# Optimization experiments

Measured on AMD Instinct MI355X. Metric: run time of the kernel, lower is better.

Reference implementation:

```python
import jax, jax.numpy as jnp
import numpy as np

N = 2060          # drug-graph nodes (m_drug_d_num)
F_OUT = 901       # out_feats, forced by Linear(901*2, ...)
M = 901 + (N - 1183)  # 1778 fused node rows
E = N * 64
N_TRAIN, N_TEST = 100000, 30000
EPS = 1e-5


def setup_inputs() -> dict:
    key = jax.random.key(0)
    ks = jax.random.split(key, 30)
    f32 = jnp.float32
    inp = {
        'x_feat': jax.random.normal(ks[0], (N, N), f32),
        'mirna_feat': jax.random.normal(ks[1], (M, F_OUT), f32),
        'Wg': jax.random.normal(ks[2], (N, F_OUT), f32) * 0.02,
        'att_src': jax.random.normal(ks[3], (F_OUT,), f32) * 0.05,
        'att_dst': jax.random.normal(ks[4], (F_OUT,), f32) * 0.05,
        'gat_b': jnp.zeros((F_OUT,), f32),
        'lw1': jax.random.normal(ks[5], (1, 2), f32) * 0.5,
        'lb1': jnp.zeros((1,), f32),
        'lw2': jax.random.normal(ks[6], (2, 1), f32) * 0.5,
        'lb2': jnp.zeros((2,), f32),
        'gw1': jax.random.normal(ks[7], (1, 2), f32) * 0.5,
        'gb1': jnp.zeros((1,), f32),
        'gw2': jax.random.normal(ks[8], (2, 1), f32) * 0.5,
        'gb2': jnp.zeros((2,), f32),
        'W1': jax.random.normal(ks[9], (2 * F_OUT, 1024), f32) * 0.02,
        'b1': jnp.zeros((1024,), f32),
        'W2': jax.random.normal(ks[10], (1024, 512), f32) * 0.03,
        'b2': jnp.zeros((512,), f32),
        'W3': jax.random.normal(ks[11], (512, 64), f32) * 0.04,
        'b3': jnp.zeros((64,), f32),
        'W4': jax.random.normal(ks[12], (64, 1), f32) * 0.1,
        'b4': jnp.zeros((1,), f32),
        'edge_index': jax.random.randint(ks[13], (2, E), 0, N, jnp.int32),
        'train_sample': jax.random.randint(ks[14], (N_TRAIN, 2), 0, M, jnp.int32),
        'test_sample': jax.random.randint(ks[15], (N_TEST, 2), 0, M, jnp.int32),
    }
    return inp


def _bn(x, axes):
    # BatchNorm in train mode (fresh module: gamma=1, beta=0, biased batch var)
    mu = x.mean(axes, keepdims=True)
    var = x.var(axes, keepdims=True)
    return (x - mu) * jax.lax.rsqrt(var + EPS)


def _gat(x, Wg, att_src, att_dst, gat_b, edge_index):
    # single-head PyG-style GATConv with self loops, negative_slope=0.2
    h = x @ Wg                                         # [N, F]
    loop = jnp.arange(N, dtype=edge_index.dtype)
    src = jnp.concatenate([edge_index[0], loop])
    dst = jnp.concatenate([edge_index[1], loop])
    a_s = h @ att_src                                  # [N]
    a_d = h @ att_dst
    e = jax.nn.leaky_relu(a_s[src] + a_d[dst], 0.2)    # per-edge logits
    emax = jax.ops.segment_max(e, dst, num_segments=N)
    ex = jnp.exp(e - emax[dst])
    denom = jax.ops.segment_sum(ex, dst, num_segments=N)
    alpha = ex / denom[dst]
    out = jax.ops.segment_sum(alpha[:, None] * h[src], dst, num_segments=N) + gat_b
    return jax.nn.relu(out)                            # F.relu in MGL (MGC relu is idempotent)


def _forward(x_feat, mirna_feat, Wg, att_src, att_dst, gat_b,
             lw1, lb1, lw2, lb2, gw1, gb1, gw2, gb2,
             W1, b1, W2, b2, W3, b3, W4, b4,
             edge_index, train_sample, test_sample):
    g = _gat(x_feat, Wg, att_src, att_dst, gat_b, edge_index)      # [N, 901]
    drug_view = jnp.concatenate([g[:901], g[1183:]], axis=0)       # [M, 901]
    x = jnp.stack([drug_view, mirna_feat], axis=1)                 # [M, 2, 901]  (B=M, C=2, H=1 dropped, W=901)

    # MS_CAM (channels=2, r=2), BN in train mode
    xl = jnp.einsum('mcw,oc->mow', x, lw1) + lb1[None, :, None]    # [M, 1, 901]
    xl = jax.nn.relu(_bn(xl, (0, 2)))
    xl = jnp.einsum('mcw,oc->mow', xl, lw2) + lb2[None, :, None]   # [M, 2, 901]
    xl = _bn(xl, (0, 2))

    gp = x.mean(axis=2)                                            # [M, 2] global avg pool
    xg = gp @ gw1.T + gb1                                          # [M, 1]
    xg = jax.nn.relu(_bn(xg, (0,)))
    xg = xg @ gw2.T + gb2                                          # [M, 2]
    xg = _bn(xg, (0,))

    wei = jax.nn.sigmoid(xl + xg[:, :, None])
    x = x * wei                                                    # [M, 2, 901]
    fused = (x[:, 0, :] + x[:, 1, :]) * 0.5                        # [M, 901]

    def score(pairs):
        emb = jnp.concatenate([fused[pairs[:, 0]], fused[pairs[:, 1]]], axis=1)  # [B, 1802]
        h = emb @ W1 + b1
        h = h @ W2 + b2
        h = h @ W3 + b3
        return jax.nn.sigmoid(h @ W4 + b4)

    return score(train_sample), score(test_sample)


def reference(x_feat, mirna_feat, Wg, att_src, att_dst, gat_b,
              lw1, lb1, lw2, lb2, gw1, gb1, gw2, gb2,
              W1, b1, W2, b2, W3, b3, W4, b4,
              edge_index, train_sample, test_sample):
    return _forward(x_feat, mirna_feat, Wg, att_src, att_dst, gat_b,
                    lw1, lb1, lw2, lb2, gw1, gb1, gw2, gb2,
                    W1, b1, W2, b2, W3, b3, W4, b4,
                    edge_index, train_sample, test_sample)
```

## Files before the change

kernel.cpp:

```cpp
#include <hip/hip_runtime.h>

typedef unsigned short u16;
typedef unsigned int   u32;

#define NN   2060
#define FF   901
#define HP   904
#define MM   1778
#define EE   131840
#define ETOT 133900
#define NTR  100000
#define NOUT 130000
#define MP   2112
#define KP   2080
#define NP   960
#define EPSV 1e-5f
#define NTOT 1601978.0

typedef __attribute__((ext_vector_type(4))) float f32x4;
typedef __attribute__((ext_vector_type(8))) short bf16x8;

#define GLL16(g,l) __builtin_amdgcn_global_load_lds( \
    (const __attribute__((address_space(1))) u32*)(g), \
    (__attribute__((address_space(3))) u32*)(l), 16, 0, 0)

__device__ __forceinline__ float bf2f(u16 u){ return __uint_as_float(((u32)u)<<16); }
__device__ __forceinline__ u16 f2bf(float f){
  u32 b = __float_as_uint(f);
  return (u16)((b + 0x7fffu + ((b>>16)&1u)) >> 16);
}
__device__ __forceinline__ float ldf(const void* p, size_t i, int bf){
  return bf ? bf2f(((const u16*)p)[i]) : ((const float*)p)[i];
}
__device__ __forceinline__ u16 ldb(const void* p, size_t i, int bf){
  return bf ? ((const u16*)p)[i] : f2bf(((const float*)p)[i]);
}
__device__ __forceinline__ float waveSum(float v){
  #pragma unroll
  for (int o = 32; o; o >>= 1) v += __shfl_down(v, o);
  return v;
}
__device__ __forceinline__ int waveSumI(int v){
  #pragma unroll
  for (int o = 32; o; o >>= 1) v += __shfl_down(v, o);
  return v;
}
__device__ __forceinline__ int flagWave(const u32* __restrict__ x){
  int l = threadIdx.x & 63;
  u32 w0 = x[l], w1 = x[l + 64];
  int big = (((w0 >> 7)  & 0xFFu) >= 0xC0u) + (((w0 >> 23) & 0xFFu) >= 0xC0u)
          + (((w1 >> 7)  & 0xFFu) >= 0xC0u) + (((w1 >> 23) & 0xFFu) >= 0xC0u);
  big = waveSumI(big);
  return (__shfl(big, 0) >= 8) ? 0 : 1;
}
__device__ __forceinline__ void edgeSD(const int* __restrict__ ei, int e, int& src, int& dst){
  if (e < EE){ src = ei[e]; dst = ei[EE + e]; } else { src = dst = e - EE; }
}

__global__ __launch_bounds__(256) void pad_k(const void* __restrict__ X, const void* __restrict__ Wg,
                                             const void* __restrict__ W3, const void* __restrict__ W4,
                                             const void* __restrict__ b3, const void* __restrict__ b4,
                                             const int* __restrict__ ei,
                                             u16* __restrict__ Ap, u16* __restrict__ BT,
                                             float* __restrict__ u3, float* __restrict__ cp,
                                             int* __restrict__ cnts, int* bfp){
  __shared__ u16 tt[32][33];
  int bf = flagWave((const u32*)X);
  int blk = blockIdx.x, tid = threadIdx.x;
  if (blk == 0 && tid == 0) *bfp = bf;
  if (blk < MP){
    int row = blk;
    for (int c0 = tid * 8; c0 < KP; c0 += 2048){
      u16 v[8] = {0,0,0,0,0,0,0,0};
      if (row < NN){
        if (c0 + 8 <= NN){
          if (bf){
            ushort4 t0 = *(const ushort4*)((const u16*)X + (size_t)row * NN + c0);
            ushort4 t1 = *(const ushort4*)((const u16*)X + (size_t)row * NN + c0 + 4);
            v[0]=t0.x; v[1]=t0.y; v[2]=t0.z; v[3]=t0.w;
            v[4]=t1.x; v[5]=t1.y; v[6]=t1.z; v[7]=t1.w;
          } else {
            float4 t0 = *(const float4*)((const float*)X + (size_t)row * NN + c0);
            float4 t1 = *(const float4*)((const float*)X + (size_t)row * NN + c0 + 4);
            v[0]=f2bf(t0.x); v[1]=f2bf(t0.y); v[2]=f2bf(t0.z); v[3]=f2bf(t0.w);
            v[4]=f2bf(t1.x); v[5]=f2bf(t1.y); v[6]=f2bf(t1.z); v[7]=f2bf(t1.w);
          }
        } else {
          #pragma unroll
          for (int i = 0; i < 8; ++i)
            if (c0 + i < NN) v[i] = ldb(X, (size_t)row * NN + c0 + i, bf);
        }
      }
      *(uint4*)(Ap + (size_t)row * KP + c0) = *(const uint4*)v;
    }
  } else if (blk < MP + 1950){
    int t = blk - MP;
    int kb = (t % 65) * 32, nb = (t / 65) * 32;
    int tx = tid & 31, ty = tid >> 5;
    #pragma unroll
    for (int i = 0; i < 4; ++i){
      int k = kb + ty + 8*i, n = nb + tx;
      u16 v = 0;
      if (k < NN && n < FF) v = ldb(Wg, (size_t)k * FF + n, bf);
      tt[ty + 8*i][tx] = v;
    }
    __syncthreads();
    #pragma unroll
    for (int i = 0; i < 4; ++i){
      int n = nb + ty + 8*i, k = kb + tx;
      if (n < NP && k < KP) BT[(size_t)n * KP + k] = tt[tx][ty + 8*i];
    }
  } else if (blk < MP + 1950 + 514){
    if (tid >= 64) return;
    int ob = blk - (MP + 1950);
    if (ob > 512) return;
    float s = (ob < 512) ? ldf(W3, (size_t)ob*64 + tid, bf) * ldf(W4, tid, bf)
                         : ldf(b3, tid, bf) * ldf(W4, tid, bf);
    s = waveSum(s);
    if (tid == 0){ if (ob < 512) u3[ob] = s; else cp[0] = s + ldf(b4, 0, bf); }
  } else {
    int e = (blk - (MP + 1950 + 514)) * 256 + tid;
    if (e >= ETOT) return;
    int src, dst; edgeSD(ei, e, src, dst);
    atomicAdd(&cnts[dst], 1);
  }
}

__global__ __launch_bounds__(256) void scan_k(const int* __restrict__ counts, int* __restrict__ offs,
                                              const void* __restrict__ W2, const void* __restrict__ b2,
                                              const float* __restrict__ u3, float* __restrict__ u2,
                                              float* __restrict__ cp, const int* bfp){
  int blk = blockIdx.x, tid = threadIdx.x;
  if (blk == 0){
    __shared__ int part[256];
    const int CH = (NN + 255) / 256;
    int base = tid * CH, s = 0;
    for (int i = 0; i < CH; ++i){ int idx = base + i; if (idx < NN) s += counts[idx]; }
    part[tid] = s;
    __syncthreads();
    if (tid == 0){ int run = 0; for (int i = 0; i < 256; ++i){ int v = part[i]; part[i] = run; run += v; } }
    __syncthreads();
    int run = part[tid];
    for (int i = 0; i < CH; ++i){ int idx = base + i; if (idx < NN){ offs[idx] = run; run += counts[idx]; } }
    if (tid == 255) offs[NN] = run;
  } else {
    int bf = *bfp;
    __shared__ float sh[4];
    #pragma unroll 1
    for (int r = 0; r < 2; ++r){
      int ob = (blk - 1) * 2 + r;
      if (ob <= 1024){
        float s = 0;
        if (ob < 1024){ for (int j = tid; j < 512; j += 256) s += ldf(W2, (size_t)ob*512 + j, bf) * u3[j]; }
        else          { for (int j = tid; j < 512; j += 256) s += ldf(b2, j, bf) * u3[j]; }
        s = waveSum(s);
        __syncthreads();
        if ((tid & 63) == 0) sh[tid >> 6] = s;
        __syncthreads();
        if (tid == 0){ float t = sh[0]+sh[1]+sh[2]+sh[3]; if (ob < 1024) u2[ob] = t; else cp[1] = t; }
      }
    }
  }
}

__global__ __launch_bounds__(256) void gemm_k(const u16* __restrict__ A, const u16* __restrict__ BT,
                                              u16* __restrict__ h,
                                              const void* __restrict__ W1, const void* __restrict__ b1,
                                              const float* __restrict__ u2, float* __restrict__ u1,
                                              float* __restrict__ cp, const int* bfp){
  __shared__ __align__(16) u16 sA[2][64*32];
  __shared__ __align__(16) u16 sB[2][64*32];
  __shared__ float shr[4];
  int blk = blockIdx.x, tid = threadIdx.x;
  if (blk >= 495){
    int bf = *bfp;
    #pragma unroll 1
    for (int r = 0; r < 4; ++r){
      int ob = (blk - 495) * 4 + r;
      if (ob <= 1802){
        float s = 0;
        if (ob < 1802){ for (int j = tid; j < 1024; j += 256) s += ldf(W1, (size_t)ob*1024 + j, bf) * u2[j]; }
        else          { for (int j = tid; j < 1024; j += 256) s += ldf(b1, j, bf) * u2[j]; }
        s = waveSum(s);
        __syncthreads();
        if ((tid & 63) == 0) shr[tid >> 6] = s;
        __syncthreads();
        if (tid == 0){ float t = shr[0]+shr[1]+shr[2]+shr[3]; if (ob < 1802) u1[ob] = t; else cp[2] = t; }
      }
    }
    return;
  }
  int bm = (blk % 33) * 64, bn = (blk / 33) * 64;
  int lane = tid & 63, wave = tid >> 6;
  int wm = (wave >> 1) * 32, wn = (wave & 1) * 32;
  f32x4 acc[2][2] = {};
  int srow = tid >> 2;
  int schunk = (tid & 3) ^ ((tid >> 3) & 3);
  const u16* gA = A  + (size_t)(bm + srow) * KP + schunk * 8;
  const u16* gB = BT + (size_t)(bn + srow) * KP + schunk * 8;
  int fr = lane & 15, quad = lane >> 4;
  int qs = quad ^ ((fr >> 1) & 3);
  const int KIT = KP / 32;
  GLL16(gA, &sA[0][wave * 512]);
  GLL16(gB, &sB[0][wave * 512]);
  for (int kt = 0; kt < KIT; ++kt){
    int cur = kt & 1;
    __syncthreads();
    if (kt + 1 < KIT){
      GLL16(gA + (kt + 1) * 32, &sA[cur ^ 1][wave * 512]);
      GLL16(gB + (kt + 1) * 32, &sB[cur ^ 1][wave * 512]);
    }
    bf16x8 a0 = *(const bf16x8*)&sA[cur][(wm      + fr) * 32 + qs * 8];
    bf16x8 a1 = *(const bf16x8*)&sA[cur][(wm + 16 + fr) * 32 + qs * 8];
    bf16x8 b0 = *(const bf16x8*)&sB[cur][(wn      + fr) * 32 + qs * 8];
    bf16x8 b1 = *(const bf16x8*)&sB[cur][(wn + 16 + fr) * 32 + qs * 8];
    acc[0][0] = __builtin_amdgcn_mfma_f32_16x16x32_bf16(a0, b0, acc[0][0], 0,0,0);
    acc[0][1] = __builtin_amdgcn_mfma_f32_16x16x32_bf16(a0, b1, acc[0][1], 0,0,0);
    acc[1][0] = __builtin_amdgcn_mfma_f32_16x16x32_bf16(a1, b0, acc[1][0], 0,0,0);
    acc[1][1] = __builtin_amdgcn_mfma_f32_16x16x32_bf16(a1, b1, acc[1][1], 0,0,0);
  }
  #pragma unroll
  for (int im = 0; im < 2; ++im)
    #pragma unroll
    for (int in = 0; in < 2; ++in)
      #pragma unroll
      for (int i = 0; i < 4; ++i){
        int row = bm + wm + im*16 + quad*4 + i;
        int col = bn + wn + in*16 + fr;
        if (row < NN && col < FF) h[(size_t)row * HP + col] = f2bf(acc[im][in][i]);
      }
}

__global__ __launch_bounds__(256) void asd_k(const u16* __restrict__ h, const void* att_s, const void* att_d,
                                             float* a_s, float* a_d, const int* bfp){
  int bf = *bfp;
  int wv = threadIdx.x >> 6, lane = threadIdx.x & 63;
  int n = blockIdx.x * 4 + wv;
  if (n >= NN) return;
  float ss = 0, sd = 0;
  for (int f = lane; f < FF; f += 64){
    float hv = bf2f(h[(size_t)n * HP + f]);
    ss += hv * ldf(att_s, f, bf);
    sd += hv * ldf(att_d, f, bf);
  }
  ss = waveSum(ss); sd = waveSum(sd);
  if (lane == 0){ a_s[n] = ss; a_d[n] = sd; }
}

__global__ __launch_bounds__(256) void edge2_k(const int* __restrict__ ei, const float* __restrict__ a_s,
                                               const float* __restrict__ a_d, float* __restrict__ denom,
                                               const int* __restrict__ offs, int* __restrict__ fill,
                                               int* __restrict__ csr_src, float* __restrict__ csr_w){
  int e = blockIdx.x * 256 + threadIdx.x;
  if (e >= ETOT) return;
  int src, dst; edgeSD(ei, e, src, dst);
  float x = a_s[src] + a_d[dst];
  float ev = x > 0.f ? x : 0.2f * x;
  float ex = expf(ev);
  atomicAdd(&denom[dst], ex);
  int pos = offs[dst] + atomicAdd(&fill[dst], 1);
  csr_src[pos] = src; csr_w[pos] = ex;
}

__device__ __forceinline__ void acc8(float* a, uint4 v, float w){
  u32 arr[4] = {v.x, v.y, v.z, v.w};
  #pragma unroll
  for (int i = 0; i < 4; ++i){
    a[2*i]   += w * __uint_as_float((arr[i] & 0xFFFFu) << 16);
    a[2*i+1] += w * __uint_as_float(arr[i] & 0xFFFF0000u);
  }
}
__global__ __launch_bounds__(128) void aggr_k(const u16* __restrict__ h, const int* __restrict__ offs,
                                              const int* __restrict__ csr_src, const float* __restrict__ csr_w,
                                              const float* __restrict__ denom, const void* gat_b,
                                              const void* __restrict__ mirna,
                                              const void* lw1, const void* lb1,
                                              float* __restrict__ g, float* __restrict__ gp,
                                              float2* __restrict__ pA, const int* bfp){
  int bf = *bfp;
  int m = blockIdx.x, tid = threadIdx.x;
  int dst = m < 901 ? m : m + 282;
  int o0 = offs[dst], o1 = offs[dst + 1];
  float inv = 1.0f / denom[dst];
  __shared__ int   sS[128];
  __shared__ float sW[128];
  __shared__ float red[4][2];
  const int c = tid;
  float a[8] = {0,0,0,0,0,0,0,0};
  for (int base = o0; base < o1; base += 128){
    int nb = min(128, o1 - base);
    __syncthreads();
    if (tid < nb){ sS[tid] = csr_src[base + tid]; sW[tid] = csr_w[base + tid] * inv; }
    __syncthreads();
    if (c < 113){
      int k = 0;
      for (; k + 4 <= nb; k += 4){
        int   i0 = sS[k], i1 = sS[k+1], i2 = sS[k+2], i3 = sS[k+3];
        float w0 = sW[k], w1 = sW[k+1], w2 = sW[k+2], w3 = sW[k+3];
        uint4 v0 = ((const uint4*)(h + (size_t)i0 * HP))[c];
        uint4 v1 = ((const uint4*)(h + (size_t)i1 * HP))[c];
        uint4 v2 = ((const uint4*)(h + (size_t)i2 * HP))[c];
        uint4 v3 = ((const uint4*)(h + (size_t)i3 * HP))[c];
        acc8(a, v0, w0); acc8(a, v1, w1); acc8(a, v2, w2); acc8(a, v3, w3);
      }
      for (; k < nb; ++k){
        uint4 v0 = ((const uint4*)(h + (size_t)sS[k] * HP))[c];
        acc8(a, v0, sW[k]);
      }
    }
  }
  float w00 = ldf(lw1,0,bf), w01 = ldf(lw1,1,bf), bb = ldf(lb1,0,bf);
  float sx0 = 0, sx1 = 0, sl = 0, sl2 = 0;
  if (c < 113){
    int f0 = 8 * c;
    float r[8];
    #pragma unroll
    for (int i = 0; i < 8; ++i){
      bool inb = (f0 + i) < FF;
      float v = a[i] + (inb ? ldf(gat_b, f0 + i, bf) : 0.f);
      v = v > 0.f ? v : 0.f;
      r[i] = inb ? v : 0.f;
      if (inb){
        float x1 = ldf(mirna, (size_t)m * FF + f0 + i, bf);
        float xl = w00*r[i] + w01*x1 + bb;
        sx0 += r[i]; sx1 += x1; sl += xl; sl2 += xl*xl;
      }
    }
    float4* go = (float4*)(g + (size_t)dst * HP);
    go[2*c]   = make_float4(r[0], r[1], r[2], r[3]);
    go[2*c+1] = make_float4(r[4], r[5], r[6], r[7]);
  }
  sx0 = waveSum(sx0); sx1 = waveSum(sx1); sl = waveSum(sl); sl2 = waveSum(sl2);
  int wv = tid >> 6;
  if ((tid & 63) == 0){ red[0][wv]=sx0; red[1][wv]=sx1; red[2][wv]=sl; red[3][wv]=sl2; }
  __syncthreads();
  if (tid == 0){
    gp[2*m]   = (red[0][0]+red[0][1]) / (float)FF;
    gp[2*m+1] = (red[1][0]+red[1][1]) / (float)FF;
    pA[m] = make_float2(red[2][0]+red[2][1], red[3][0]+red[3][1]);
  }
}

__global__ __launch_bounds__(256) void xg_k(const float* __restrict__ gp, const void* gw1, const void* gb1,
                                            const void* gw2, float* __restrict__ xg2b,
                                            const float2* __restrict__ pA, double* __restrict__ Sd,
                                            const int* bfp){
  int bf = *bfp;
  __shared__ float xs[MM];
  __shared__ float red[2][4];
  __shared__ float bc[3];
  int tid = threadIdx.x;
  float s = 0, s2 = 0;
  for (int m = tid; m < MM; m += 256){ float2 p = pA[m]; s += p.x; s2 += p.y; }
  s = waveSum(s); s2 = waveSum(s2);
  if ((tid & 63) == 0){ red[0][tid>>6] = s; red[1][tid>>6] = s2; }
  __syncthreads();
  if (tid == 0){
    Sd[0] = (double)(red[0][0]+red[0][1]+red[0][2]+red[0][3]);
    Sd[1] = (double)(red[1][0]+red[1][1]+red[1][2]+red[1][3]);
  }
  __syncthreads();
  float g10 = ldf(gw1,0,bf), g11 = ldf(gw1,1,bf), b1v = ldf(gb1,0,bf);
  s = 0; s2 = 0;
  for (int m = tid; m < MM; m += 256){
    float v = g10*gp[2*m] + g11*gp[2*m+1] + b1v;
    xs[m] = v; s += v; s2 += v*v;
  }
  s = waveSum(s); s2 = waveSum(s2);
  __syncthreads();
  if ((tid & 63) == 0){ red[0][tid>>6] = s; red[1][tid>>6] = s2; }
  __syncthreads();
  if (tid == 0){
    float t  = red[0][0]+red[0][1]+red[0][2]+red[0][3];
    float t2 = red[1][0]+red[1][1]+red[1][2]+red[1][3];
    float mean = t / (float)MM, var = t2 / (float)MM - mean*mean;
    bc[0] = mean; bc[1] = rsqrtf(var + EPSV);
  }
  __syncthreads();
  float mean = bc[0], rs = bc[1];
  s = 0; s2 = 0;
  for (int m = tid; m < MM; m += 256){
    float r = (xs[m] - mean) * rs; r = r > 0.f ? r : 0.f;
    xs[m] = r; s += r; s2 += r*r;
  }
  s = waveSum(s); s2 = waveSum(s2);
  __syncthreads();
  if ((tid & 63) == 0){ red[0][tid>>6] = s; red[1][tid>>6] = s2; }
  __syncthreads();
  if (tid == 0){
    float t  = red[0][0]+red[0][1]+red[0][2]+red[0][3];
    float t2 = red[1][0]+red[1][1]+red[1][2]+red[1][3];
    float mrg = t / (float)MM, vrg = t2 / (float)MM - mrg*mrg;
    float g20 = ldf(gw2,0,bf), g21 = ldf(gw2,1,bf);
    bc[0] = mrg;
    bc[1] = g20 * rsqrtf(g20*g20*vrg + EPSV);
    bc[2] = g21 * rsqrtf(g21*g21*vrg + EPSV);
  }
  __syncthreads();
  float mrg = bc[0], c0 = bc[1], c1 = bc[2];
  for (int m = tid; m < MM; m += 256){
    float d = xs[m] - mrg;
    xg2b[2*m] = c0 * d; xg2b[2*m+1] = c1 * d;
  }
}

__global__ __launch_bounds__(256) void statsB_k(const float* __restrict__ g, const void* __restrict__ mirna,
                                                const void* lw1, const void* lb1,
                                                const double* __restrict__ S, float2* __restrict__ pB,
                                                const int* bfp){
  int bf = *bfp;
  int m = blockIdx.x, tid = threadIdx.x;
  int gr = m < 901 ? m : m + 282;
  float w00 = ldf(lw1,0,bf), w01 = ldf(lw1,1,bf), bb = ldf(lb1,0,bf);
  float mu1 = (float)(S[0] / NTOT);
  float rs1 = rsqrtf((float)(S[1] / NTOT) - mu1*mu1 + EPSV);
  float sr = 0, sr2 = 0;
  for (int w = tid; w < FF; w += 256){
    float x0 = g[(size_t)gr * HP + w];
    float x1 = ldf(mirna, (size_t)m * FF + w, bf);
    float xl = w00*x0 + w01*x1 + bb;
    float r = (xl - mu1) * rs1; r = r > 0.f ? r : 0.f;
    sr += r; sr2 += r*r;
  }
  sr = waveSum(sr); sr2 = waveSum(sr2);
  __shared__ float sh[2][4];
  if ((tid & 63) == 0){ sh[0][tid>>6] = sr; sh[1][tid>>6] = sr2; }
  __syncthreads();
  if (tid == 0) pB[m] = make_float2(sh[0][0]+sh[0][1]+sh[0][2]+sh[0][3],
                                    sh[1][0]+sh[1][1]+sh[1][2]+sh[1][3]);
}

__global__ __launch_bounds__(256) void redB_k(const float2* __restrict__ pB, double* __restrict__ Sd){
  int tid = threadIdx.x;
  float s = 0, s2 = 0;
  for (int m = tid; m < MM; m += 256){ float2 p = pB[m]; s += p.x; s2 += p.y; }
  s = waveSum(s); s2 = waveSum(s2);
  __shared__ float sh[2][4];
  if ((tid & 63) == 0){ sh[0][tid>>6] = s; sh[1][tid>>6] = s2; }
  __syncthreads();
  if (tid == 0){
    Sd[2] = (double)(sh[0][0]+sh[0][1]+sh[0][2]+sh[0][3]);
    Sd[3] = (double)(sh[1][0]+sh[1][1]+sh[1][2]+sh[1][3]);
  }
}

__global__ __launch_bounds__(256) void fs_k(const float* __restrict__ g, const void* __restrict__ mirna,
                                            const void* lw1, const void* lb1, const void* lw2,
                                            const double* __restrict__ S, const float* __restrict__ xg2b,
                                            const float* __restrict__ u1,
                                            float* __restrict__ s0, float* __restrict__ s1, const int* bfp){
  int bf = *bfp;
  int m = blockIdx.x, tid = threadIdx.x;
  int gr = m < 901 ? m : m + 282;
  float w00 = ldf(lw1,0,bf), w01 = ldf(lw1,1,bf), bb = ldf(lb1,0,bf);
  float mu1 = (float)(S[0] / NTOT);
  float rs1 = rsqrtf((float)(S[1] / NTOT) - mu1*mu1 + EPSV);
  float mr  = (float)(S[2] / NTOT);
  float vr  = (float)(S[3] / NTOT) - mr*mr;
  float l20 = ldf(lw2,0,bf), l21 = ldf(lw2,1,bf);
  float A0 = l20 * rsqrtf(l20*l20*vr + EPSV);
  float A1 = l21 * rsqrtf(l21*l21*vr + EPSV);
  float xa = xg2b[2*m], xb = xg2b[2*m+1];
  float p0 = 0, p1 = 0;
  for (int w = tid; w < FF; w += 256){
    float x0 = g[(size_t)gr * HP + w];
    float x1 = ldf(mirna, (size_t)m * FF + w, bf);
    float xl = w00*x0 + w01*x1 + bb;
    float r = (xl - mu1) * rs1; r = r > 0.f ? r : 0.f;
    float rc = r - mr;
    float z0 = A0*rc + xa, z1 = A1*rc + xb;
    float sg0 = 1.f / (1.f + expf(-z0));
    float sg1 = 1.f / (1.f + expf(-z1));
    float f = 0.5f * (x0*sg0 + x1*sg1);
    p0 += f * u1[w]; p1 += f * u1[901 + w];
  }
  p0 = waveSum(p0); p1 = waveSum(p1);
  __shared__ float sh[2][4];
  if ((tid & 63) == 0){ sh[0][tid>>6] = p0; sh[1][tid>>6] = p1; }
  __syncthreads();
  if (tid == 0){
    s0[m] = sh[0][0]+sh[0][1]+sh[0][2]+sh[0][3];
    s1[m] = sh[1][0]+sh[1][1]+sh[1][2]+sh[1][3];
  }
}

__global__ __launch_bounds__(256) void out_k(const int* __restrict__ tr, const int* __restrict__ te,
                                             const float* __restrict__ s0, const float* __restrict__ s1,
                                             const float* __restrict__ cp, void* __restrict__ out,
                                             const int* bfp){
  int bf = *bfp;
  int b = blockIdx.x * 256 + threadIdx.x;
  if (b >= NOUT) return;
  int i, j;
  if (b < NTR){ i = tr[2*b]; j = tr[2*b + 1]; }
  else { int t = b - NTR; i = te[2*t]; j = te[2*t + 1]; }
  float z = s0[i] + s1[j] + cp[0] + cp[1] + cp[2];
  float v = 1.f / (1.f + expf(-z));
  if (bf) ((u16*)out)[b] = f2bf(v);
  else    ((float*)out)[b] = v;
}

extern "C" void kernel_launch(void* const* d_in, const int* in_sizes, int n_in,
                              void* d_out, int out_size, void* d_ws, size_t ws_size,
                              hipStream_t stream){
  const void* x_feat = d_in[0];
  const void* mirna  = d_in[1];
  const void* Wg     = d_in[2];
  const void* att_s  = d_in[3];
  const void* att_d  = d_in[4];
  const void* gat_b  = d_in[5];
  const void* lw1    = d_in[6];
  const void* lb1    = d_in[7];
  const void* lw2    = d_in[8];
  const void* gw1    = d_in[10];
  const void* gb1    = d_in[11];
  const void* gw2    = d_in[12];
  const void* W1     = d_in[14];
  const void* b1     = d_in[15];
  const void* W2     = d_in[16];
  const void* b2     = d_in[17];
  const void* W3     = d_in[18];
  const void* b3     = d_in[19];
  const void* W4     = d_in[20];
  const void* b4     = d_in[21];
  const int* ei      = (const int*)d_in[22];
  const int* tr      = (const int*)d_in[23];
  const int* te      = (const int*)d_in[24];

  char* ws = (char*)d_ws;
  size_t off = 0;
  auto alloc = [&](size_t bytes)->size_t{ size_t o = off; off += (bytes + 255) & ~(size_t)255; return o; };
  size_t oA  = alloc((size_t)MP*KP*2);
  size_t oBT = alloc((size_t)NP*KP*2);
  size_t oH  = alloc((size_t)NN*HP*2);
  size_t oCS = alloc((size_t)ETOT*4);
  size_t oCW = alloc((size_t)ETOT*4);
  size_t oAS = alloc(NN*4);
  size_t oAD = alloc(NN*4);
  size_t oOF = alloc((NN+1)*4);
  size_t oGP = alloc(MM*2*4);
  size_t oXG = alloc(MM*2*4);
  size_t oS0 = alloc(MM*4);
  size_t oS1 = alloc(MM*4);
  size_t oU3 = alloc(512*4);
  size_t oU2 = alloc(1024*4);
  size_t oU1 = alloc(1802*4);
  size_t oPA = alloc(MM*8);
  size_t oPB = alloc(MM*8);
  size_t oSS = alloc(4*8);
  size_t oCP = alloc(3*4);
  size_t oBF = alloc(4);
  size_t zstart = off;
  size_t oCT = alloc(NN*4);
  size_t oFL = alloc(NN*4);
  size_t oDN = alloc(NN*4);
  size_t zend = off;

  u16*   Ap   = (u16*)(ws+oA);
  u16*   BT   = (u16*)(ws+oBT);
  u16*   h    = (u16*)(ws+oH);
  float* gbuf = (float*)(ws+oA);
  int*   csrS = (int*)(ws+oCS);
  float* csrW = (float*)(ws+oCW);
  float* a_s  = (float*)(ws+oAS);
  float* a_d  = (float*)(ws+oAD);
  int*   offs = (int*)(ws+oOF);
  float* gp   = (float*)(ws+oGP);
  float* xg2b = (float*)(ws+oXG);
  float* s0   = (float*)(ws+oS0);
  float* s1   = (float*)(ws+oS1);
  float* u3   = (float*)(ws+oU3);
  float* u2   = (float*)(ws+oU2);
  float* u1   = (float*)(ws+oU1);
  float2* pA  = (float2*)(ws+oPA);
  float2* pB  = (float2*)(ws+oPB);
  double* Sd  = (double*)(ws+oSS);
  float* cp   = (float*)(ws+oCP);
  int*   bfp  = (int*)(ws+oBF);
  int*   cnts = (int*)(ws+oCT);
  int*   fill = (int*)(ws+oFL);
  float* denom= (float*)(ws+oDN);

  hipMemsetAsync(ws + zstart, 0, zend - zstart, stream);

  pad_k  <<<MP + 1950 + 514 + (ETOT+255)/256, 256, 0, stream>>>(
      x_feat, Wg, W3, W4, b3, b4, ei, Ap, BT, u3, cp, cnts, bfp);
  scan_k <<<514, 256, 0, stream>>>(cnts, offs, W2, b2, u3, u2, cp, bfp);
  gemm_k <<<495 + 451, 256, 0, stream>>>(Ap, BT, h, W1, b1, u2, u1, cp, bfp);
  asd_k  <<<(NN+3)/4, 256, 0, stream>>>(h, att_s, att_d, a_s, a_d, bfp);
  edge2_k<<<(ETOT+255)/256, 256, 0, stream>>>(ei, a_s, a_d, denom, offs, fill, csrS, csrW);
  aggr_k <<<MM, 128, 0, stream>>>(h, offs, csrS, csrW, denom, gat_b, mirna, lw1, lb1, gbuf, gp, pA, bfp);
  xg_k   <<<1, 256, 0, stream>>>(gp, gw1, gb1, gw2, xg2b, pA, Sd, bfp);
  statsB_k<<<MM, 256, 0, stream>>>(gbuf, mirna, lw1, lb1, Sd, pB, bfp);
  redB_k <<<1, 256, 0, stream>>>(pB, Sd);
  fs_k   <<<MM, 256, 0, stream>>>(gbuf, mirna, lw1, lb1, lw2, Sd, xg2b, u1, s0, s1, bfp);
  out_k  <<<(NOUT+255)/256, 256, 0, stream>>>(tr, te, s0, s1, cp, d_out, bfp);
}
```

Baseline: 259.4 us.

## Merge small tail and mid kernels into persistent kernels with grid barriers

Replaces the asd/edge kernels and the five tail kernels (xg, statsB, redB, fs, out) with two persistent 512-block kernels. They use a software grid barrier built on atomics. The tail kernel keeps each block's g and mirna rows in shared memory across phases, so they are not re-read from global memory. This removes several launch gaps and one global re-read. It risks deadlock if all 512 blocks are not co-resident, and the barrier spin adds latency.

```diff
diff --git a/kernel.cpp b/kernel.cpp
--- a/kernel.cpp
+++ b/kernel.cpp
@@ -16,6 +16,7 @@
 #define NP   960
 #define EPSV 1e-5f
 #define NTOT 1601978.0
+#define GRD  512
 
 typedef __attribute__((ext_vector_type(4))) float f32x4;
 typedef __attribute__((ext_vector_type(8))) short bf16x8;
@@ -55,6 +56,26 @@
 }
 __device__ __forceinline__ void edgeSD(const int* __restrict__ ei, int e, int& src, int& dst){
   if (e < EE){ src = ei[e]; dst = ei[EE + e]; } else { src = dst = e - EE; }
+}
+
+__device__ __forceinline__ void gbar(int* cnt, int* gen){
+  __syncthreads();
+  if (threadIdx.x == 0){
+    __threadfence();
+    int g = atomicAdd(gen, 0);
+    if (atomicAdd(cnt, 1) == GRD - 1){
+      atomicExch(cnt, 0);
+      __threadfence();
+      atomicAdd(gen, 1);
+    } else {
+      for (long it = 0; it < (1L << 22); ++it){
+        if (atomicAdd(gen, 0) != g) break;
+        __builtin_amdgcn_s_sleep(8);
+      }
+    }
+    __threadfence();
+  }
+  __syncthreads();
 }
 
 __global__ __launch_bounds__(256) void pad_k(const void* __restrict__ X, const void* __restrict__ Wg,
@@ -231,35 +252,36 @@
       }
 }
 
-__global__ __launch_bounds__(256) void asd_k(const u16* __restrict__ h, const void* att_s, const void* att_d,
-                                             float* a_s, float* a_d, const int* bfp){
-  int bf = *bfp;
-  int wv = threadIdx.x >> 6, lane = threadIdx.x & 63;
-  int n = blockIdx.x * 4 + wv;
-  if (n >= NN) return;
-  float ss = 0, sd = 0;
-  for (int f = lane; f < FF; f += 64){
-    float hv = bf2f(h[(size_t)n * HP + f]);
-    ss += hv * ldf(att_s, f, bf);
-    sd += hv * ldf(att_d, f, bf);
-  }
-  ss = waveSum(ss); sd = waveSum(sd);
-  if (lane == 0){ a_s[n] = ss; a_d[n] = sd; }
-}
-
-__global__ __launch_bounds__(256) void edge2_k(const int* __restrict__ ei, const float* __restrict__ a_s,
-                                               const float* __restrict__ a_d, float* __restrict__ denom,
-                                               const int* __restrict__ offs, int* __restrict__ fill,
-                                               int* __restrict__ csr_src, float* __restrict__ csr_w){
-  int e = blockIdx.x * 256 + threadIdx.x;
-  if (e >= ETOT) return;
-  int src, dst; edgeSD(ei, e, src, dst);
-  float x = a_s[src] + a_d[dst];
-  float ev = x > 0.f ? x : 0.2f * x;
-  float ex = expf(ev);
-  atomicAdd(&denom[dst], ex);
-  int pos = offs[dst] + atomicAdd(&fill[dst], 1);
-  csr_src[pos] = src; csr_w[pos] = ex;
+__global__ __launch_bounds__(256, 2) void mid_k(const u16* __restrict__ h, const void* att_s, const void* att_d,
+                                                const int* __restrict__ ei,
+                                                float* __restrict__ a_s, float* __restrict__ a_d,
+                                                float* __restrict__ denom, const int* __restrict__ offs,
+                                                int* __restrict__ fill, int* __restrict__ csrS,
+                                                float* __restrict__ csrW, const int* bfp, int* bar){
+  int blk = blockIdx.x, tid = threadIdx.x, bf = *bfp;
+  {
+    int wv = tid >> 6, lane = tid & 63;
+    for (int n = blk * 4 + wv; n < NN; n += GRD * 4){
+      float ss = 0, sd = 0;
+      for (int f = lane; f < FF; f += 64){
+        float hv = bf2f(h[(size_t)n * HP + f]);
+        ss += hv * ldf(att_s, f, bf);
+        sd += hv * ldf(att_d, f, bf);
+      }
+      ss = waveSum(ss); sd = waveSum(sd);
+      if (lane == 0){ a_s[n] = ss; a_d[n] = sd; }
+    }
+  }
+  gbar(&bar[0], &bar[1]);
+  for (int e = blk * 256 + tid; e < ETOT; e += GRD * 256){
+    int src, dst; edgeSD(ei, e, src, dst);
+    float x = a_s[src] + a_d[dst];
+    float ev = x > 0.f ? x : 0.2f * x;
+    float ex = expf(ev);
+    atomicAdd(&denom[dst], ex);
+    int pos = offs[dst] + atomicAdd(&fill[dst], 1);
+    csrS[pos] = src; csrW[pos] = ex;
+  }
 }
 
 __device__ __forceinline__ void acc8(float* a, uint4 v, float w){
@@ -341,163 +363,174 @@
   }
 }
 
-__global__ __launch_bounds__(256) void xg_k(const float* __restrict__ gp, const void* gw1, const void* gb1,
-                                            const void* gw2, float* __restrict__ xg2b,
-                                            const float2* __restrict__ pA, double* __restrict__ Sd,
-                                            const int* bfp){
-  int bf = *bfp;
+__global__ __launch_bounds__(256, 2) void tail_k(
+    const float* __restrict__ g, const void* __restrict__ mirna,
+    const void* lw1, const void* lb1, const void* lw2,
+    const void* gw1, const void* gb1, const void* gw2,
+    const float* __restrict__ u1, const int* __restrict__ tr, const int* __restrict__ te,
+    const float* __restrict__ cp, const float* __restrict__ gp,
+    const float2* __restrict__ pA, float2* __restrict__ pB,
+    double* __restrict__ SdA, double* __restrict__ SdB,
+    float* __restrict__ xg2b, float* __restrict__ s0, float* __restrict__ s1,
+    void* __restrict__ out, const int* bfp, int* bar)
+{
+  __shared__ float xr[4][FF];
+  __shared__ float yr[4][FF];
   __shared__ float xs[MM];
-  __shared__ float red[2][4];
+  __shared__ float sred[2][4];
   __shared__ float bc[3];
-  int tid = threadIdx.x;
-  float s = 0, s2 = 0;
-  for (int m = tid; m < MM; m += 256){ float2 p = pA[m]; s += p.x; s2 += p.y; }
-  s = waveSum(s); s2 = waveSum(s2);
-  if ((tid & 63) == 0){ red[0][tid>>6] = s; red[1][tid>>6] = s2; }
-  __syncthreads();
-  if (tid == 0){
-    Sd[0] = (double)(red[0][0]+red[0][1]+red[0][2]+red[0][3]);
-    Sd[1] = (double)(red[1][0]+red[1][1]+red[1][2]+red[1][3]);
-  }
-  __syncthreads();
-  float g10 = ldf(gw1,0,bf), g11 = ldf(gw1,1,bf), b1v = ldf(gb1,0,bf);
-  s = 0; s2 = 0;
-  for (int m = tid; m < MM; m += 256){
-    float v = g10*gp[2*m] + g11*gp[2*m+1] + b1v;
-    xs[m] = v; s += v; s2 += v*v;
-  }
-  s = waveSum(s); s2 = waveSum(s2);
-  __syncthreads();
-  if ((tid & 63) == 0){ red[0][tid>>6] = s; red[1][tid>>6] = s2; }
-  __syncthreads();
-  if (tid == 0){
-    float t  = red[0][0]+red[0][1]+red[0][2]+red[0][3];
-    float t2 = red[1][0]+red[1][1]+red[1][2]+red[1][3];
-    float mean = t / (float)MM, var = t2 / (float)MM - mean*mean;
-    bc[0] = mean; bc[1] = rsqrtf(var + EPSV);
-  }
-  __syncthreads();
-  float mean = bc[0], rs = bc[1];
-  s = 0; s2 = 0;
-  for (int m = tid; m < MM; m += 256){
-    float r = (xs[m] - mean) * rs; r = r > 0.f ? r : 0.f;
-    xs[m] = r; s += r; s2 += r*r;
-  }
-  s = waveSum(s); s2 = waveSum(s2);
-  __syncthreads();
-  if ((tid & 63) == 0){ red[0][tid>>6] = s; red[1][tid>>6] = s2; }
-  __syncthreads();
-  if (tid == 0){
-    float t  = red[0][0]+red[0][1]+red[0][2]+red[0][3];
-    float t2 = red[1][0]+red[1][1]+red[1][2]+red[1][3];
-    float mrg = t / (float)MM, vrg = t2 / (float)MM - mrg*mrg;
-    float g20 = ldf(gw2,0,bf), g21 = ldf(gw2,1,bf);
-    bc[0] = mrg;
-    bc[1] = g20 * rsqrtf(g20*g20*vrg + EPSV);
-    bc[2] = g21 * rsqrtf(g21*g21*vrg + EPSV);
-  }
-  __syncthreads();
-  float mrg = bc[0], c0 = bc[1], c1 = bc[2];
-  for (int m = tid; m < MM; m += 256){
-    float d = xs[m] - mrg;
-    xg2b[2*m] = c0 * d; xg2b[2*m+1] = c1 * d;
-  }
-}
-
-__global__ __launch_bounds__(256) void statsB_k(const float* __restrict__ g, const void* __restrict__ mirna,
-                                                const void* lw1, const void* lb1,
-                                                const double* __restrict__ S, float2* __restrict__ pB,
-                                                const int* bfp){
-  int bf = *bfp;
-  int m = blockIdx.x, tid = threadIdx.x;
-  int gr = m < 901 ? m : m + 282;
+  int blk = blockIdx.x, tid = threadIdx.x, bf = *bfp;
+  int wv = tid >> 6;
   float w00 = ldf(lw1,0,bf), w01 = ldf(lw1,1,bf), bb = ldf(lb1,0,bf);
-  float mu1 = (float)(S[0] / NTOT);
-  float rs1 = rsqrtf((float)(S[1] / NTOT) - mu1*mu1 + EPSV);
-  float sr = 0, sr2 = 0;
-  for (int w = tid; w < FF; w += 256){
-    float x0 = g[(size_t)gr * HP + w];
-    float x1 = ldf(mirna, (size_t)m * FF + w, bf);
-    float xl = w00*x0 + w01*x1 + bb;
-    float r = (xl - mu1) * rs1; r = r > 0.f ? r : 0.f;
-    sr += r; sr2 += r*r;
-  }
-  sr = waveSum(sr); sr2 = waveSum(sr2);
-  __shared__ float sh[2][4];
-  if ((tid & 63) == 0){ sh[0][tid>>6] = sr; sh[1][tid>>6] = sr2; }
-  __syncthreads();
-  if (tid == 0) pB[m] = make_float2(sh[0][0]+sh[0][1]+sh[0][2]+sh[0][3],
-                                    sh[1][0]+sh[1][1]+sh[1][2]+sh[1][3]);
-}
-
-__global__ __launch_bounds__(256) void redB_k(const float2* __restrict__ pB, double* __restrict__ Sd){
-  int tid = threadIdx.x;
-  float s = 0, s2 = 0;
-  for (int m = tid; m < MM; m += 256){ float2 p = pB[m]; s += p.x; s2 += p.y; }
-  s = waveSum(s); s2 = waveSum(s2);
-  __shared__ float sh[2][4];
-  if ((tid & 63) == 0){ sh[0][tid>>6] = s; sh[1][tid>>6] = s2; }
-  __syncthreads();
-  if (tid == 0){
-    Sd[2] = (double)(sh[0][0]+sh[0][1]+sh[0][2]+sh[0][3]);
-    Sd[3] = (double)(sh[1][0]+sh[1][1]+sh[1][2]+sh[1][3]);
-  }
-}
-
-__global__ __launch_bounds__(256) void fs_k(const float* __restrict__ g, const void* __restrict__ mirna,
-                                            const void* lw1, const void* lb1, const void* lw2,
-                                            const double* __restrict__ S, const float* __restrict__ xg2b,
-                                            const float* __restrict__ u1,
-                                            float* __restrict__ s0, float* __restrict__ s1, const int* bfp){
-  int bf = *bfp;
-  int m = blockIdx.x, tid = threadIdx.x;
-  int gr = m < 901 ? m : m + 282;
-  float w00 = ldf(lw1,0,bf), w01 = ldf(lw1,1,bf), bb = ldf(lb1,0,bf);
-  float mu1 = (float)(S[0] / NTOT);
-  float rs1 = rsqrtf((float)(S[1] / NTOT) - mu1*mu1 + EPSV);
-  float mr  = (float)(S[2] / NTOT);
-  float vr  = (float)(S[3] / NTOT) - mr*mr;
-  float l20 = ldf(lw2,0,bf), l21 = ldf(lw2,1,bf);
-  float A0 = l20 * rsqrtf(l20*l20*vr + EPSV);
-  float A1 = l21 * rsqrtf(l21*l21*vr + EPSV);
-  float xa = xg2b[2*m], xb = xg2b[2*m+1];
-  float p0 = 0, p1 = 0;
-  for (int w = tid; w < FF; w += 256){
-    float x0 = g[(size_t)gr * HP + w];
-    float x1 = ldf(mirna, (size_t)m * FF + w, bf);
-    float xl = w00*x0 + w01*x1 + bb;
-    float r = (xl - mu1) * rs1; r = r > 0.f ? r : 0.f;
-    float rc = r - mr;
-    float z0 = A0*rc + xa, z1 = A1*rc + xb;
-    float sg0 = 1.f / (1.f + expf(-z0));
-    float sg1 = 1.f / (1.f + expf(-z1));
-    float f = 0.5f * (x0*sg0 + x1*sg1);
-    p0 += f * u1[w]; p1 += f * u1[901 + w];
-  }
-  p0 = waveSum(p0); p1 = waveSum(p1);
-  __shared__ float sh[2][4];
-  if ((tid & 63) == 0){ sh[0][tid>>6] = p0; sh[1][tid>>6] = p1; }
-  __syncthreads();
-  if (tid == 0){
-    s0[m] = sh[0][0]+sh[0][1]+sh[0][2]+sh[0][3];
-    s1[m] = sh[1][0]+sh[1][1]+sh[1][2]+sh[1][3];
-  }
-}
-
-__global__ __launch_bounds__(256) void out_k(const int* __restrict__ tr, const int* __restrict__ te,
-                                             const float* __restrict__ s0, const float* __restrict__ s1,
-                                             const float* __restrict__ cp, void* __restrict__ out,
-                                             const int* bfp){
-  int bf = *bfp;
-  int b = blockIdx.x * 256 + threadIdx.x;
-  if (b >= NOUT) return;
-  int i, j;
-  if (b < NTR){ i = tr[2*b]; j = tr[2*b + 1]; }
-  else { int t = b - NTR; i = te[2*t]; j = te[2*t + 1]; }
-  float z = s0[i] + s1[j] + cp[0] + cp[1] + cp[2];
-  float v = 1.f / (1.f + expf(-z));
-  if (bf) ((u16*)out)[b] = f2bf(v);
-  else    ((float*)out)[b] = v;
+
+  if (blk == 0){
+    float s = 0, s2 = 0;
+    for (int m = tid; m < MM; m += 256){ float2 p = pA[m]; s += p.x; s2 += p.y; }
+    s = waveSum(s); s2 = waveSum(s2);
+    if ((tid & 63) == 0){ sred[0][wv] = s; sred[1][wv] = s2; }
+    __syncthreads();
+    if (tid == 0){
+      SdA[0] = (double)(sred[0][0]+sred[0][1]+sred[0][2]+sred[0][3]);
+      SdA[1] = (double)(sred[1][0]+sred[1][1]+sred[1][2]+sred[1][3]);
+    }
+    __syncthreads();
+    float g10 = ldf(gw1,0,bf), g11 = ldf(gw1,1,bf), b1v = ldf(gb1,0,bf);
+    s = 0; s2 = 0;
+    for (int m = tid; m < MM; m += 256){
+      float v = g10*gp[2*m] + g11*gp[2*m+1] + b1v;
+      xs[m] = v; s += v; s2 += v*v;
+    }
+    s = waveSum(s); s2 = waveSum(s2);
+    __syncthreads();
+    if ((tid & 63) == 0){ sred[0][wv] = s; sred[1][wv] = s2; }
+    __syncthreads();
+    if (tid == 0){
+      float t  = sred[0][0]+sred[0][1]+sred[0][2]+sred[0][3];
+      float t2 = sred[1][0]+sred[1][1]+sred[1][2]+sred[1][3];
+      float mean = t / (float)MM, var = t2 / (float)MM - mean*mean;
+      bc[0] = mean; bc[1] = rsqrtf(var + EPSV);
+    }
+    __syncthreads();
+    float mean = bc[0], rs = bc[1];
+    s = 0; s2 = 0;
+    for (int m = tid; m < MM; m += 256){
+      float r = (xs[m] - mean) * rs; r = r > 0.f ? r : 0.f;
+      xs[m] = r; s += r; s2 += r*r;
+    }
+    s = waveSum(s); s2 = waveSum(s2);
+    __syncthreads();
+    if ((tid & 63) == 0){ sred[0][wv] = s; sred[1][wv] = s2; }
+    __syncthreads();
+    if (tid == 0){
+      float t  = sred[0][0]+sred[0][1]+sred[0][2]+sred[0][3];
+      float t2 = sred[1][0]+sred[1][1]+sred[1][2]+sred[1][3];
+      float mrg = t / (float)MM, vrg = t2 / (float)MM - mrg*mrg;
+      float g20 = ldf(gw2,0,bf), g21 = ldf(gw2,1,bf);
+      bc[0] = mrg;
+      bc[1] = g20 * rsqrtf(g20*g20*vrg + EPSV);
+      bc[2] = g21 * rsqrtf(g21*g21*vrg + EPSV);
+    }
+    __syncthreads();
+    float mrg = bc[0], c0 = bc[1], c1 = bc[2];
+    for (int m = tid; m < MM; m += 256){
+      float d = xs[m] - mrg;
+      xg2b[2*m] = c0 * d; xg2b[2*m+1] = c1 * d;
+    }
+  }
+  #pragma unroll 1
+  for (int r = 0; r < 4; ++r){
+    int m = blk + GRD * r;
+    if (m >= MM) break;
+    int gr = m < 901 ? m : m + 282;
+    for (int w = tid; w < FF; w += 256){
+      xr[r][w] = g[(size_t)gr * HP + w];
+      yr[r][w] = ldf(mirna, (size_t)m * FF + w, bf);
+    }
+  }
+  gbar(&bar[0], &bar[1]);
+
+  float mu1 = (float)(SdA[0] / NTOT);
+  float rs1 = rsqrtf((float)(SdA[1] / NTOT) - mu1*mu1 + EPSV);
+  #pragma unroll 1
+  for (int r = 0; r < 4; ++r){
+    int m = blk + GRD * r;
+    if (m >= MM) break;
+    float sr = 0, sr2 = 0;
+    for (int w = tid; w < FF; w += 256){
+      float xl = w00*xr[r][w] + w01*yr[r][w] + bb;
+      float rr = (xl - mu1) * rs1; rr = rr > 0.f ? rr : 0.f;
+      sr += rr; sr2 += rr*rr;
+    }
+    sr = waveSum(sr); sr2 = waveSum(sr2);
+    __syncthreads();
+    if ((tid & 63) == 0){ sred[0][wv] = sr; sred[1][wv] = sr2; }
+    __syncthreads();
+    if (tid == 0) pB[m] = make_float2(sred[0][0]+sred[0][1]+sred[0][2]+sred[0][3],
+                                      sred[1][0]+sred[1][1]+sred[1][2]+sred[1][3]);
+  }
+  gbar(&bar[0], &bar[1]);
+
+  if (blk == 0){
+    float s = 0, s2 = 0;
+    for (int m = tid; m < MM; m += 256){ float2 p = pB[m]; s += p.x; s2 += p.y; }
+    s = waveSum(s); s2 = waveSum(s2);
+    __syncthreads();
+    if ((tid & 63) == 0){ sred[0][wv] = s; sred[1][wv] = s2; }
+    __syncthreads();
+    if (tid == 0){
+      SdB[0] = (double)(sred[0][0]+sred[0][1]+sred[0][2]+sred[0][3]);
+      SdB[1] = (double)(sred[1][0]+sred[1][1]+sred[1][2]+sred[1][3]);
+    }
+  }
+  gbar(&bar[0], &bar[1]);
+
+  {
+    float mr = (float)(SdB[0] / NTOT);
+    float vr = (float)(SdB[1] / NTOT) - mr*mr;
+    float l20 = ldf(lw2,0,bf), l21 = ldf(lw2,1,bf);
+    float A0 = l20 * rsqrtf(l20*l20*vr + EPSV);
+    float A1 = l21 * rsqrtf(l21*l21*vr + EPSV);
+    #pragma unroll 1
+    for (int r = 0; r < 4; ++r){
+      int m = blk + GRD * r;
+      if (m >= MM) break;
+      float xa = xg2b[2*m], xb = xg2b[2*m+1];
+      float p0 = 0, p1 = 0;
+      for (int w = tid; w < FF; w += 256){
+        float x0 = xr[r][w], x1 = yr[r][w];
+        float xl = w00*x0 + w01*x1 + bb;
+        float rr = (xl - mu1) * rs1; rr = rr > 0.f ? rr : 0.f;
+        float rc = rr - mr;
+        float z0 = A0*rc + xa, z1 = A1*rc + xb;
+        float sg0 = 1.f / (1.f + expf(-z0));
+        float sg1 = 1.f / (1.f + expf(-z1));
+        float f = 0.5f * (x0*sg0 + x1*sg1);
+        p0 += f * u1[w]; p1 += f * u1[901 + w];
+      }
+      p0 = waveSum(p0); p1 = waveSum(p1);
+      __syncthreads();
+      if ((tid & 63) == 0){ sred[0][wv] = p0; sred[1][wv] = p1; }
+      __syncthreads();
+      if (tid == 0){
+        s0[m] = sred[0][0]+sred[0][1]+sred[0][2]+sred[0][3];
+        s1[m] = sred[1][0]+sred[1][1]+sred[1][2]+sred[1][3];
+      }
+    }
+  }
+  gbar(&bar[0], &bar[1]);
+
+  {
+    float cc = cp[0] + cp[1] + cp[2];
+    for (int b = blk * 256 + tid; b < NOUT; b += GRD * 256){
+      int i, j;
+      if (b < NTR){ i = tr[2*b]; j = tr[2*b + 1]; }
+      else { int t = b - NTR; i = te[2*t]; j = te[2*t + 1]; }
+      float z = s0[i] + s1[j] + cc;
+      float v = 1.f / (1.f + expf(-z));
+      if (bf) ((u16*)out)[b] = f2bf(v);
+      else    ((float*)out)[b] = v;
+    }
+  }
 }
 
 extern "C" void kernel_launch(void* const* d_in, const int* in_sizes, int n_in,
@@ -547,13 +580,15 @@
   size_t oU1 = alloc(1802*4);
   size_t oPA = alloc(MM*8);
   size_t oPB = alloc(MM*8);
-  size_t oSS = alloc(4*8);
+  size_t oSA = alloc(2*8);
+  size_t oSB = alloc(2*8);
   size_t oCP = alloc(3*4);
   size_t oBF = alloc(4);
   size_t zstart = off;
   size_t oCT = alloc(NN*4);
   size_t oFL = alloc(NN*4);
   size_t oDN = alloc(NN*4);
+  size_t oBR = alloc(4*4);
   size_t zend = off;
 
   u16*   Ap   = (u16*)(ws+oA);
@@ -574,12 +609,15 @@
   float* u1   = (float*)(ws+oU1);
   float2* pA  = (float2*)(ws+oPA);
   float2* pB  = (float2*)(ws+oPB);
-  double* Sd  = (double*)(ws+oSS);
+  double* SdA = (double*)(ws+oSA);
+  double* SdB = (double*)(ws+oSB);
   float* cp   = (float*)(ws+oCP);
   int*   bfp  = (int*)(ws+oBF);
   int*   cnts = (int*)(ws+oCT);
   int*   fill = (int*)(ws+oFL);
   float* denom= (float*)(ws+oDN);
+  int*   barM = (int*)(ws+oBR);
+  int*   barT = (int*)(ws+oBR+8);
 
   hipMemsetAsync(ws + zstart, 0, zend - zstart, stream);
 
@@ -587,12 +625,8 @@
       x_feat, Wg, W3, W4, b3, b4, ei, Ap, BT, u3, cp, cnts, bfp);
   scan_k <<<514, 256, 0, stream>>>(cnts, offs, W2, b2, u3, u2, cp, bfp);
   gemm_k <<<495 + 451, 256, 0, stream>>>(Ap, BT, h, W1, b1, u2, u1, cp, bfp);
-  asd_k  <<<(NN+3)/4, 256, 0, stream>>>(h, att_s, att_d, a_s, a_d, bfp);
-  edge2_k<<<(ETOT+255)/256, 256, 0, stream>>>(ei, a_s, a_d, denom, offs, fill, csrS, csrW);
+  mid_k  <<<GRD, 256, 0, stream>>>(h, att_s, att_d, ei, a_s, a_d, denom, offs, fill, csrS, csrW, bfp, barM);
   aggr_k <<<MM, 128, 0, stream>>>(h, offs, csrS, csrW, denom, gat_b, mirna, lw1, lb1, gbuf, gp, pA, bfp);
-  xg_k   <<<1, 256, 0, stream>>>(gp, gw1, gb1, gw2, xg2b, pA, Sd, bfp);
-  statsB_k<<<MM, 256, 0, stream>>>(gbuf, mirna, lw1, lb1, Sd, pB, bfp);
-  redB_k <<<1, 256, 0, stream>>>(pB, Sd);
-  fs_k   <<<MM, 256, 0, stream>>>(gbuf, mirna, lw1, lb1, lw2, Sd, xg2b, u1, s0, s1, bfp);
-  out_k  <<<(NOUT+255)/256, 256, 0, stream>>>(tr, te, s0, s1, cp, d_out, bfp);
-}
+  tail_k <<<GRD, 256, 0, stream>>>(gbuf, mirna, lw1, lb1, lw2, gw1, gb1, gw2, u1, tr, te,
+                                   cp, gp, pA, pB, SdA, SdB, xg2b, s0, s1, d_out, bfp, barT);
+}
```

New measurement: 455.2 us. 75.5% more time.
